# Kernel tuning notes

Hardware: AMD Instinct MI355X
Metric: run time of the kernel (lower is better)

The kernel has to match this reference:

```python
import jax, jax.numpy as jnp
import numpy as np

B, S, D = 16, 2048, 128
NEG = -1000000000.0


def setup_inputs() -> dict:
    key = jax.random.key(0)
    kq, kk, kv = jax.random.split(key, 3)
    q = jax.random.normal(kq, (B, S, D), dtype=jnp.float32)
    k = jax.random.normal(kk, (B, S, D), dtype=jnp.float32)
    v = jax.random.normal(kv, (B, S, D), dtype=jnp.float32)
    # causal mask: True entries are masked out (filled with -1e9)
    mask = jnp.broadcast_to(
        jnp.triu(jnp.ones((S, S), dtype=bool), k=1)[None, :, :], (B, S, S)
    )
    return {"q": q, "k": k, "v": v, "mask": mask}


def reference(q, k, v, mask):
    # attn = q @ k^T / sqrt(d_k), masked_fill, softmax over keys, attn @ v
    scale = jnp.sqrt(jnp.asarray(D, dtype=q.dtype))
    attn = jnp.einsum("bqd,bkd->bqk", q, k) / scale
    attn = jnp.where(mask, jnp.asarray(NEG, dtype=attn.dtype), attn)
    attn = jax.nn.softmax(attn, axis=2)
    out = jnp.einsum("bqk,bkd->bqd", attn, v)
    return (out, attn)
```

## Files before the change

kernel.cpp:

```cpp
#include <hip/hip_runtime.h>

#define B_ 16
#define S_ 2048
#define D_ 128

typedef __attribute__((ext_vector_type(8))) short bf16x8;
typedef __attribute__((ext_vector_type(4))) float f32x4;
typedef __attribute__((ext_vector_type(16))) float f32x16;
typedef __attribute__((ext_vector_type(2))) unsigned int u32x2;
typedef __attribute__((ext_vector_type(4))) unsigned int u32x4;

__device__ __forceinline__ unsigned short f2bf(float f) {
    unsigned int u = __builtin_bit_cast(unsigned int, f);
    u += 0x7fff + ((u >> 16) & 1);
    return (unsigned short)(u >> 16);
}

__device__ __forceinline__ void gload16(const void* g, void* l) {
    __builtin_amdgcn_global_load_lds(
        (const __attribute__((address_space(1))) void*)g,
        (__attribute__((address_space(3))) void*)l, 16, 0, 0);
}

#define WAITV(n) asm volatile("s_waitcnt vmcnt(" #n ")" ::: "memory")

__global__ __launch_bounds__(256, 4)
void conv_kv(const float* __restrict__ kg, const float* __restrict__ vg,
             char* __restrict__ kws, char* __restrict__ vws, float* __restrict__ attng)
{
    __shared__ float lt[64 * 132];
    const int bid = blockIdx.x;
    const int tid = threadIdx.x;
    if (bid < 512) {
        const int b = bid >> 5, t = bid & 31;
        const float* src = kg + ((long)bid << 13);
        char* dst = kws + ((long)bid << 14);
#pragma unroll
        for (int it = 0; it < 4; ++it) {
            const int c = tid + it * 256;
            const int r = c >> 4, j = c & 15;
            f32x4 a = *(const f32x4*)(src + r * 128 + j * 8);
            f32x4 cc = *(const f32x4*)(src + r * 128 + j * 8 + 4);
            u32x4 p;
            p[0] = (unsigned)f2bf(a[0]) | ((unsigned)f2bf(a[1]) << 16);
            p[1] = (unsigned)f2bf(a[2]) | ((unsigned)f2bf(a[3]) << 16);
            p[2] = (unsigned)f2bf(cc[0]) | ((unsigned)f2bf(cc[1]) << 16);
            p[3] = (unsigned)f2bf(cc[2]) | ((unsigned)f2bf(cc[3]) << 16);
            *(u32x4*)(dst + r * 256 + ((j ^ (r & 7)) << 4)) = p;
        }
        const f32x4 z = {0.f, 0.f, 0.f, 0.f};
        {
            const int W4 = (31 - t) * 16;
            float* base = attng + ((long)(b * S_) + t * 64) * S_ + (t + 1) * 64;
            for (int row = 0; row < 32; ++row) {
                float* rb = base + (long)row * S_;
                for (int c = tid; c < W4; c += 256)
                    *(f32x4*)(rb + c * 4) = z;
            }
        }
        {
            const int s = 31 - t;
            const int W4 = t * 16;
            float* base = attng + ((long)(b * S_) + s * 64 + 32) * S_ + (s + 1) * 64;
            for (int row = 0; row < 32; ++row) {
                float* rb = base + (long)row * S_;
                for (int c = tid; c < W4; c += 256)
                    *(f32x4*)(rb + c * 4) = z;
            }
        }
    } else {
        const int vb = bid - 512;
        const float* src = vg + ((long)vb << 13);
        char* dst = vws + ((long)vb << 14);
#pragma unroll
        for (int it = 0; it < 8; ++it) {
            const int c = tid + it * 256;
            const int r = c >> 5, q = c & 31;
            *(f32x4*)(lt + r * 132 + q * 4) = *(const f32x4*)(src + r * 128 + q * 4);
        }
        __syncthreads();
#pragma unroll
        for (int it = 0; it < 4; ++it) {
            const int c = tid + it * 256;
            const int d = c >> 3, jc = c & 7;
            unsigned short e[8];
#pragma unroll
            for (int ee = 0; ee < 8; ++ee) e[ee] = f2bf(lt[(jc * 8 + ee) * 132 + d]);
            u32x4 p;
            p[0] = (unsigned)e[0] | ((unsigned)e[1] << 16);
            p[1] = (unsigned)e[2] | ((unsigned)e[3] << 16);
            p[2] = (unsigned)e[4] | ((unsigned)e[5] << 16);
            p[3] = (unsigned)e[6] | ((unsigned)e[7] << 16);
            *(u32x4*)(dst + d * 128 + ((jc ^ (d & 7)) << 4)) = p;
        }
    }
}

__device__ __forceinline__ int qtile_of(int b, int t) {
    const int f = (t & 1) ? (t >> 1) : (31 - (t >> 1));
    return (b & 8) ? (31 - f) : f;
}

__global__ __launch_bounds__(256, 2)
void flash_fused(const float* __restrict__ qg, const char* __restrict__ kws,
                 const char* __restrict__ vws,
                 float* __restrict__ outg, float* __restrict__ attng)
{
    __shared__ char lds[65536];

    const int tid = threadIdx.x, lane = tid & 63, w = tid >> 6;
    const int wq = w >> 1, wk = w & 1;
    const int l31 = lane & 31, hi = lane >> 5;
    const int bid = blockIdx.x;
    const int b = bid >> 5;
    const int qt = qtile_of(b, bid & 31);
    const int q0 = qt * 64;
    const int nt = qt + 1;
    const float scale = 0.088388347648318447f;
    const int qrow = q0 + wq * 32 + l31;

    bf16x8 qf[8];
    {
        const float* qr = qg + ((long)b * S_ + qrow) * D_;
#pragma unroll
        for (int km = 0; km < 8; ++km) {
            const int d0 = km * 16 + hi * 8;
            f32x4 a = *(const f32x4*)(qr + d0);
            f32x4 c = *(const f32x4*)(qr + d0 + 4);
            bf16x8 t;
            t[0] = (short)f2bf(a[0]); t[1] = (short)f2bf(a[1]);
            t[2] = (short)f2bf(a[2]); t[3] = (short)f2bf(a[3]);
            t[4] = (short)f2bf(c[0]); t[5] = (short)f2bf(c[1]);
            t[6] = (short)f2bf(c[2]); t[7] = (short)f2bf(c[3]);
            qf[km] = t;
        }
    }
    WAITV(0);

    const char* kb0 = kws + ((long)(b * 32) << 14);
    const char* vb0 = vws + ((long)(b * 32) << 14);

    const int krow = wk * 32 + l31;
    const int krb = krow * 256;
    const int ksw = krow & 7;

#pragma unroll
    for (int it = 0; it < 4; ++it)
        gload16(kb0 + it * 4096 + tid * 16, lds + it * 4096 + tid * 16);

    float sumA = 0.f;
    int buf = 0;
    for (int kt = 0; kt < nt; ++kt) {
        const bool pf = (kt + 1 < nt);
        if (pf) {
            const char* kn = kb0 + ((long)(kt + 1) << 14);
            const int db = (buf ^ 1) * 16384;
#pragma unroll
            for (int it = 0; it < 4; ++it)
                gload16(kn + it * 4096 + tid * 16, lds + db + it * 4096 + tid * 16);
            WAITV(4);
        } else {
            WAITV(0);
        }
        __builtin_amdgcn_s_barrier();
        __builtin_amdgcn_sched_barrier(0);

        const char* kbuf = lds + buf * 16384;
        f32x16 acc;
#pragma unroll
        for (int i = 0; i < 16; ++i) acc[i] = 0.f;
        __builtin_amdgcn_s_setprio(1);
#pragma unroll
        for (int km = 0; km < 8; ++km) {
            bf16x8 kf = *(const bf16x8*)(kbuf + krb + (((km * 2 + hi) ^ ksw) << 4));
            acc = __builtin_amdgcn_mfma_f32_32x32x16_bf16(kf, qf[km], acc, 0, 0, 0);
        }
        __builtin_amdgcn_s_setprio(0);

        const int kbase = kt * 64 + wk * 32;
#pragma unroll
        for (int r = 0; r < 16; ++r) {
            const int kl = (r & 3) + 8 * (r >> 2) + 4 * hi;
            if (kbase + kl <= qrow) sumA += __expf(acc[r] * scale);
        }
        __builtin_amdgcn_sched_barrier(0);
        __builtin_amdgcn_s_barrier();
        buf ^= 1;
    }

    sumA += __shfl_xor(sumA, 32, 64);
    float* sums = (float*)lds;
    if (!hi) sums[(wq * 2 + wk) * 32 + l31] = sumA;
    __syncthreads();
    const float invl_l = 1.f / (sums[(wq * 2 + 0) * 32 + l31] + sums[(wq * 2 + 1) * 32 + l31]);
    __syncthreads();

    f32x16 oacc[4];
#pragma unroll
    for (int dt = 0; dt < 4; ++dt)
#pragma unroll
        for (int i = 0; i < 16; ++i) oacc[dt][i] = 0.f;

    float* attn_row = attng + ((long)b * S_ + qrow) * S_;

#pragma unroll
    for (int it = 0; it < 4; ++it)
        gload16(kb0 + it * 4096 + tid * 16, lds + it * 4096 + tid * 16);
#pragma unroll
    for (int it = 0; it < 4; ++it)
        gload16(vb0 + it * 4096 + tid * 16, lds + 32768 + it * 4096 + tid * 16);

    buf = 0;
    for (int kt = 0; kt < nt; ++kt) {
        const bool pf = (kt + 1 < nt);
        if (pf) {
            const char* kn = kb0 + ((long)(kt + 1) << 14);
            const char* vn = vb0 + ((long)(kt + 1) << 14);
            const int db = (buf ^ 1) * 16384;
#pragma unroll
            for (int it = 0; it < 4; ++it)
                gload16(kn + it * 4096 + tid * 16, lds + db + it * 4096 + tid * 16);
#pragma unroll
            for (int it = 0; it < 4; ++it)
                gload16(vn + it * 4096 + tid * 16, lds + 32768 + db + it * 4096 + tid * 16);
        }
        if (kt == 0) { if (pf) { WAITV(8); } else { WAITV(0); } }
        else         { if (pf) { WAITV(12); } else { WAITV(4); } }
        __builtin_amdgcn_s_barrier();
        __builtin_amdgcn_sched_barrier(0);

        const char* kbuf = lds + buf * 16384;
        const char* vbuf = lds + 32768 + buf * 16384;

        f32x16 acc;
#pragma unroll
        for (int i = 0; i < 16; ++i) acc[i] = 0.f;
        __builtin_amdgcn_s_setprio(1);
#pragma unroll
        for (int km = 0; km < 8; ++km) {
            bf16x8 kf = *(const bf16x8*)(kbuf + krb + (((km * 2 + hi) ^ ksw) << 4));
            acc = __builtin_amdgcn_mfma_f32_32x32x16_bf16(kf, qf[km], acc, 0, 0, 0);
        }
        __builtin_amdgcn_s_setprio(0);

        const int kbase = kt * 64 + wk * 32;
        unsigned W[8], PW[8];
#pragma unroll
        for (int i = 0; i < 8; ++i) {
            const int r0 = 2 * i;
            const int kl0 = (r0 & 3) + 8 * (r0 >> 2) + 4 * hi;
            const float p0 = (kbase + kl0 > qrow) ? 0.f : __expf(acc[r0] * scale);
            const float p1 = (kbase + kl0 + 1 > qrow) ? 0.f : __expf(acc[r0 + 1] * scale);
            W[i] = (unsigned)f2bf(p0) | ((unsigned)f2bf(p1) << 16);
        }
#pragma unroll
        for (int i = 0; i < 8; ++i)
            PW[i] = (unsigned)__shfl_xor((int)W[i], 32, 64);

        bf16x8 pa[2];
        float* arow = attn_row + kbase;
#pragma unroll
        for (int kc = 0; kc < 2; ++kc) {
            u32x4 fr;
            fr[0] = hi ? PW[kc * 4 + 2] : W[kc * 4 + 0];
            fr[1] = hi ? PW[kc * 4 + 3] : W[kc * 4 + 1];
            fr[2] = hi ? W[kc * 4 + 2] : PW[kc * 4 + 0];
            fr[3] = hi ? W[kc * 4 + 3] : PW[kc * 4 + 1];
            pa[kc] = __builtin_bit_cast(bf16x8, fr);
            f32x4 s0, s1;
            s0[0] = __builtin_bit_cast(float, fr[0] << 16) * invl_l;
            s0[1] = __builtin_bit_cast(float, fr[0] & 0xffff0000u) * invl_l;
            s0[2] = __builtin_bit_cast(float, fr[1] << 16) * invl_l;
            s0[3] = __builtin_bit_cast(float, fr[1] & 0xffff0000u) * invl_l;
            s1[0] = __builtin_bit_cast(float, fr[2] << 16) * invl_l;
            s1[1] = __builtin_bit_cast(float, fr[2] & 0xffff0000u) * invl_l;
            s1[2] = __builtin_bit_cast(float, fr[3] << 16) * invl_l;
            s1[3] = __builtin_bit_cast(float, fr[3] & 0xffff0000u) * invl_l;
            *(f32x4*)(arow + kc * 16 + hi * 8) = s0;
            *(f32x4*)(arow + kc * 16 + hi * 8 + 4) = s1;
        }

        __builtin_amdgcn_s_setprio(1);
#pragma unroll
        for (int dt = 0; dt < 4; ++dt) {
            const int d = dt * 32 + l31;
            const int rowb = d * 128;
            const int sw = (d & 7) << 4;
#pragma unroll
            for (int kc = 0; kc < 2; ++kc) {
                const int jc = wk * 4 + kc * 2 + hi;
                bf16x8 vf = *(const bf16x8*)(vbuf + rowb + ((jc << 4) ^ sw));
                oacc[dt] = __builtin_amdgcn_mfma_f32_32x32x16_bf16(pa[kc], vf, oacc[dt], 0, 0, 0);
            }
        }
        __builtin_amdgcn_s_setprio(0);
        __builtin_amdgcn_sched_barrier(0);
        __builtin_amdgcn_s_barrier();
        buf ^= 1;
    }

    __syncthreads();
    float* red = (float*)lds;
    if (wk) {
#pragma unroll
        for (int dt = 0; dt < 4; ++dt)
#pragma unroll
            for (int r = 0; r < 16; ++r) {
                const int qr = (r & 3) + 8 * (r >> 2) + 4 * hi;
                red[wq * 4096 + qr * 128 + dt * 32 + l31] = oacc[dt][r];
            }
    }
    __syncthreads();
    if (!wk) {
        float iv[16];
#pragma unroll
        for (int r = 0; r < 16; ++r) {
            const int qr = (r & 3) + 8 * (r >> 2) + 4 * hi;
            iv[r] = __shfl(invl_l, qr, 64);
        }
        float* ob = outg + ((long)b * S_ + q0 + wq * 32) * D_;
#pragma unroll
        for (int dt = 0; dt < 4; ++dt)
#pragma unroll
            for (int r = 0; r < 16; ++r) {
                const int qr = (r & 3) + 8 * (r >> 2) + 4 * hi;
                ob[(long)qr * D_ + dt * 32 + l31] =
                    (oacc[dt][r] + red[wq * 4096 + qr * 128 + dt * 32 + l31]) * iv[r];
            }
    }
}

__global__ __launch_bounds__(256, 2)
void attn_fallback(const float* __restrict__ qg, const float* __restrict__ kg,
                   const float* __restrict__ vg,
                   float* __restrict__ outg, float* __restrict__ attng)
{
    __shared__ unsigned short kT[64 * 128];
    __shared__ unsigned short vT[128 * 64];
    __shared__ unsigned short pT[4][16 * 64];
    const int tid = threadIdx.x, lane = tid & 63, w = tid >> 6;
    const int l15 = lane & 15, l4 = lane >> 4;
    const int bid = blockIdx.x;
    const int b = bid >> 5, qt = 31 - (bid & 31), q0 = qt * 64;
    const float scale = 0.088388347648318447f;
    bf16x8 qf[4];
    {
        const float* qrow = qg + ((long)b * S_ + q0 + w * 16 + l15) * D_;
#pragma unroll
        for (int kk = 0; kk < 4; ++kk) {
            const int d0 = kk * 32 + l4 * 8;
            f32x4 a = *(const f32x4*)(qrow + d0);
            f32x4 c = *(const f32x4*)(qrow + d0 + 4);
            bf16x8 t;
            t[0] = (short)f2bf(a[0]); t[1] = (short)f2bf(a[1]);
            t[2] = (short)f2bf(a[2]); t[3] = (short)f2bf(a[3]);
            t[4] = (short)f2bf(c[0]); t[5] = (short)f2bf(c[1]);
            t[6] = (short)f2bf(c[2]); t[7] = (short)f2bf(c[3]);
            qf[kk] = t;
        }
    }
    float m[4], l[4];
#pragma unroll
    for (int r = 0; r < 4; ++r) { m[r] = -1e30f; l[r] = 0.f; }
    for (int kt = 0; kt <= qt; ++kt) {
        __syncthreads();
        {
            const float* kbase = kg + ((long)b * S_ + kt * 64) * D_;
#pragma unroll
            for (int it = 0; it < 8; ++it) {
                const int c = tid + it * 256, row = c >> 5, dc = c & 31;
                f32x4 a = *(const f32x4*)(kbase + row * D_ + dc * 4);
                u32x2 p;
                p[0] = (unsigned)f2bf(a[0]) | ((unsigned)f2bf(a[1]) << 16);
                p[1] = (unsigned)f2bf(a[2]) | ((unsigned)f2bf(a[3]) << 16);
                *(u32x2*)((char*)kT + row * 256 + ((dc * 8) ^ ((row & 7) << 4))) = p;
            }
        }
        __syncthreads();
        f32x4 acc[4];
#pragma unroll
        for (int n = 0; n < 4; ++n) {
            f32x4 a = {0.f, 0.f, 0.f, 0.f};
            const int krow = n * 16 + l15, rb = krow * 256, swz = (krow & 7) << 4;
#pragma unroll
            for (int kk = 0; kk < 4; ++kk) {
                bf16x8 bf = *(const bf16x8*)((const char*)kT + rb + ((l4 * 16 + kk * 64) ^ swz));
                a = __builtin_amdgcn_mfma_f32_16x16x32_bf16(qf[kk], bf, a, 0, 0, 0);
            }
            acc[n] = a;
        }
        const bool diag = (kt == qt);
        float tm[4] = {-3e38f, -3e38f, -3e38f, -3e38f};
#pragma unroll
        for (int n = 0; n < 4; ++n)
#pragma unroll
            for (int r = 0; r < 4; ++r) {
                float s = acc[n][r] * scale;
                if (diag && (n * 16 + l15 > w * 16 + l4 * 4 + r)) s = -3e38f;
                acc[n][r] = s; tm[r] = fmaxf(tm[r], s);
            }
#pragma unroll
        for (int off = 1; off < 16; off <<= 1)
#pragma unroll
            for (int r = 0; r < 4; ++r) tm[r] = fmaxf(tm[r], __shfl_xor(tm[r], off, 64));
        float sum[4], mn[4];
#pragma unroll
        for (int r = 0; r < 4; ++r) {
            mn[r] = fmaxf(m[r], tm[r]);
            float s0 = 0.f;
#pragma unroll
            for (int n = 0; n < 4; ++n) s0 += __expf(acc[n][r] - mn[r]);
            sum[r] = s0;
        }
#pragma unroll
        for (int off = 1; off < 16; off <<= 1)
#pragma unroll
            for (int r = 0; r < 4; ++r) sum[r] += __shfl_xor(sum[r], off, 64);
#pragma unroll
        for (int r = 0; r < 4; ++r) { l[r] = l[r] * __expf(m[r] - mn[r]) + sum[r]; m[r] = mn[r]; }
    }
    float invl[4];
#pragma unroll
    for (int r = 0; r < 4; ++r) invl[r] = 1.f / l[r];
    f32x4 oacc[8];
#pragma unroll
    for (int n = 0; n < 8; ++n) oacc[n] = (f32x4){0.f, 0.f, 0.f, 0.f};
    float* attn_base = attng + ((long)b * S_ + q0) * S_;
    for (int kt = 0; kt <= qt; ++kt) {
        __syncthreads();
        {
            const float* kbase = kg + ((long)b * S_ + kt * 64) * D_;
#pragma unroll
            for (int it = 0; it < 8; ++it) {
                const int c = tid + it * 256, row = c >> 5, dc = c & 31;
                f32x4 a = *(const f32x4*)(kbase + row * D_ + dc * 4);
                u32x2 p;
                p[0] = (unsigned)f2bf(a[0]) | ((unsigned)f2bf(a[1]) << 16);
                p[1] = (unsigned)f2bf(a[2]) | ((unsigned)f2bf(a[3]) << 16);
                *(u32x2*)((char*)kT + row * 256 + ((dc * 8) ^ ((row & 7) << 4))) = p;
            }
        }
        {
            const float* vbase = vg + ((long)b * S_ + kt * 64) * D_;
#pragma unroll
            for (int it = 0; it < 8; ++it) {
                const int c = tid + it * 256, kr = c & 63, dq = c >> 6;
                f32x4 a = *(const f32x4*)(vbase + kr * D_ + dq * 4);
#pragma unroll
                for (int j = 0; j < 4; ++j) {
                    const int d = dq * 4 + j;
                    *(unsigned short*)((char*)vT + d * 128 + ((kr * 2) ^ ((d & 7) << 4))) = f2bf(a[j]);
                }
            }
        }
        __syncthreads();
        f32x4 acc[4];
#pragma unroll
        for (int n = 0; n < 4; ++n) {
            f32x4 a = {0.f, 0.f, 0.f, 0.f};
            const int krow = n * 16 + l15, rb = krow * 256, swz = (krow & 7) << 4;
#pragma unroll
            for (int kk = 0; kk < 4; ++kk) {
                bf16x8 bf = *(const bf16x8*)((const char*)kT + rb + ((l4 * 16 + kk * 64) ^ swz));
                a = __builtin_amdgcn_mfma_f32_16x16x32_bf16(qf[kk], bf, a, 0, 0, 0);
            }
            acc[n] = a;
        }
        const bool diag = (kt == qt);
#pragma unroll
        for (int n = 0; n < 4; ++n)
#pragma unroll
            for (int r = 0; r < 4; ++r) {
                float s = acc[n][r] * scale;
                if (diag && (n * 16 + l15 > w * 16 + l4 * 4 + r)) s = -3e38f;
                const float p = __expf(s - m[r]) * invl[r];
                attn_base[(long)(w * 16 + l4 * 4 + r) * S_ + kt * 64 + n * 16 + l15] = p;
                const int prow = l4 * 4 + r;
                *(unsigned short*)((char*)&pT[w][0] + prow * 128 + ((n * 32 + l15 * 2) ^ ((prow & 7) << 4))) = f2bf(p);
            }
        asm volatile("s_waitcnt lgkmcnt(0)" ::: "memory");
        __builtin_amdgcn_sched_barrier(0);
        bf16x8 pa[2];
#pragma unroll
        for (int kk = 0; kk < 2; ++kk)
            pa[kk] = *(const bf16x8*)((const char*)&pT[w][0] + l15 * 128 + ((l4 * 16 + kk * 64) ^ ((l15 & 7) << 4)));
#pragma unroll
        for (int n = 0; n < 8; ++n) {
            const int vrow = n * 16 + l15, rb = vrow * 128, swz = (vrow & 7) << 4;
#pragma unroll
            for (int kk = 0; kk < 2; ++kk) {
                bf16x8 bv = *(const bf16x8*)((const char*)vT + rb + ((l4 * 16 + kk * 64) ^ swz));
                oacc[n] = __builtin_amdgcn_mfma_f32_16x16x32_bf16(pa[kk], bv, oacc[n], 0, 0, 0);
            }
        }
    }
    {
        float* obase = outg + ((long)b * S_ + q0 + w * 16) * D_;
#pragma unroll
        for (int n = 0; n < 8; ++n)
#pragma unroll
            for (int r = 0; r < 4; ++r)
                obase[(long)(l4 * 4 + r) * D_ + n * 16 + l15] = oacc[n][r];
    }
    {
        const int col0 = (qt + 1) * 64;
        if (col0 < S_) {
            const int nch = (S_ - col0) >> 2;
            const f32x4 z = {0.f, 0.f, 0.f, 0.f};
            for (int row = w; row < 64; row += 4) {
                float* rbase = attn_base + (long)row * S_ + col0;
                for (int c = lane; c < nch; c += 64)
                    *(f32x4*)(rbase + c * 4) = z;
            }
        }
    }
}

extern "C" void kernel_launch(void* const* d_in, const int* in_sizes, int n_in,
                              void* d_out, int out_size, void* d_ws, size_t ws_size,
                              hipStream_t stream) {
    const float* q = (const float*)d_in[0];
    const float* k = (const float*)d_in[1];
    const float* v = (const float*)d_in[2];
    float* out  = (float*)d_out;
    float* attn = out + (long)B_ * S_ * D_;
    const size_t NEED = 2u * 8388608u;
    if (ws_size >= NEED) {
        char* kws = (char*)d_ws;
        char* vws = kws + 8388608;
        conv_kv<<<dim3(1024), dim3(256), 0, stream>>>(k, v, kws, vws, attn);
        flash_fused<<<dim3(512), dim3(256), 0, stream>>>(q, kws, vws, out, attn);
    } else {
        attn_fallback<<<dim3(512), dim3(256), 0, stream>>>(q, k, v, out, attn);
    }
}
```

Before: 122.3 us.

## Single-pass flash with unnormalized bf16 P workspace and separate expand kernel

Replaces the two-pass attention (a QK pass for row sums, then a second QK pass that writes normalized attn and accumulates PV) with one pass. That pass stores the unnormalized bf16 probabilities to a workspace, accumulates PV, and writes the per-row inverse sums. A new expand kernel then reads the bf16 P, scales it by the inverse sum and writes the fp32 attn matrix. This removes the redundant QK^T recompute and K reload. In exchange it adds an extra workspace write and read of P and a third kernel launch, and the new path is used only when the workspace is large enough.

```diff
diff --git a/kernel.cpp b/kernel.cpp
--- a/kernel.cpp
+++ b/kernel.cpp
@@ -23,6 +23,8 @@
 }
 
 #define WAITV(n) asm volatile("s_waitcnt vmcnt(" #n ")" ::: "memory")
+
+#define PB 4325376L
 
 __global__ __launch_bounds__(256, 4)
 void conv_kv(const float* __restrict__ kg, const float* __restrict__ vg,
@@ -102,9 +104,9 @@
 }
 
 __global__ __launch_bounds__(256, 2)
-void flash_fused(const float* __restrict__ qg, const char* __restrict__ kws,
-                 const char* __restrict__ vws,
-                 float* __restrict__ outg, float* __restrict__ attng)
+void flash_p(const float* __restrict__ qg, const char* __restrict__ kws,
+             const char* __restrict__ vws, float* __restrict__ lg,
+             char* __restrict__ pws, float* __restrict__ outg)
 {
     __shared__ char lds[65536];
 
@@ -118,6 +120,7 @@
     const int nt = qt + 1;
     const float scale = 0.088388347648318447f;
     const int qrow = q0 + wq * 32 + l31;
+    const int lr = wq * 32 + l31;
 
     bf16x8 qf[8];
     {
@@ -137,8 +140,17 @@
     }
     WAITV(0);
 
+    f32x16 oacc[4];
+#pragma unroll
+    for (int dt = 0; dt < 4; ++dt)
+#pragma unroll
+        for (int i = 0; i < 16; ++i) oacc[dt][i] = 0.f;
+    float sumA = 0.f;
+
     const char* kb0 = kws + ((long)(b * 32) << 14);
     const char* vb0 = vws + ((long)(b * 32) << 14);
+    char* pbase = pws + (long)b * PB + 4096L * qt * (qt + 1);
+    const int prstride = nt * 128;
 
     const int krow = wk * 32 + l31;
     const int krb = krow * 256;
@@ -147,7 +159,204 @@
 #pragma unroll
     for (int it = 0; it < 4; ++it)
         gload16(kb0 + it * 4096 + tid * 16, lds + it * 4096 + tid * 16);
-
+#pragma unroll
+    for (int it = 0; it < 4; ++it)
+        gload16(vb0 + it * 4096 + tid * 16, lds + 32768 + it * 4096 + tid * 16);
+
+    int buf = 0;
+    for (int kt = 0; kt < nt; ++kt) {
+        const bool pf = (kt + 1 < nt);
+        if (pf) {
+            const char* kn = kb0 + ((long)(kt + 1) << 14);
+            const char* vn = vb0 + ((long)(kt + 1) << 14);
+            const int db = (buf ^ 1) * 16384;
+#pragma unroll
+            for (int it = 0; it < 4; ++it)
+                gload16(kn + it * 4096 + tid * 16, lds + db + it * 4096 + tid * 16);
+#pragma unroll
+            for (int it = 0; it < 4; ++it)
+                gload16(vn + it * 4096 + tid * 16, lds + 32768 + db + it * 4096 + tid * 16);
+        }
+        if (kt == 0) { if (pf) { WAITV(8); } else { WAITV(0); } }
+        else         { if (pf) { WAITV(10); } else { WAITV(2); } }
+        __builtin_amdgcn_s_barrier();
+        __builtin_amdgcn_sched_barrier(0);
+
+        const char* kbuf = lds + buf * 16384;
+        const char* vbuf = lds + 32768 + buf * 16384;
+
+        f32x16 acc;
+#pragma unroll
+        for (int i = 0; i < 16; ++i) acc[i] = 0.f;
+        __builtin_amdgcn_s_setprio(1);
+#pragma unroll
+        for (int km = 0; km < 8; ++km) {
+            bf16x8 kf = *(const bf16x8*)(kbuf + krb + (((km * 2 + hi) ^ ksw) << 4));
+            acc = __builtin_amdgcn_mfma_f32_32x32x16_bf16(kf, qf[km], acc, 0, 0, 0);
+        }
+        __builtin_amdgcn_s_setprio(0);
+
+        const int kbase = kt * 64 + wk * 32;
+        unsigned W[8], PW[8];
+#pragma unroll
+        for (int i = 0; i < 8; ++i) {
+            const int r0 = 2 * i;
+            const int kl0 = (r0 & 3) + 8 * (r0 >> 2) + 4 * hi;
+            const float p0 = (kbase + kl0 > qrow) ? 0.f : __expf(acc[r0] * scale);
+            const float p1 = (kbase + kl0 + 1 > qrow) ? 0.f : __expf(acc[r0 + 1] * scale);
+            sumA += p0 + p1;
+            W[i] = (unsigned)f2bf(p0) | ((unsigned)f2bf(p1) << 16);
+        }
+#pragma unroll
+        for (int i = 0; i < 8; ++i)
+            PW[i] = (unsigned)__shfl_xor((int)W[i], 32, 64);
+
+        bf16x8 pa[2];
+#pragma unroll
+        for (int kc = 0; kc < 2; ++kc) {
+            u32x4 fr;
+            fr[0] = hi ? PW[kc * 4 + 2] : W[kc * 4 + 0];
+            fr[1] = hi ? PW[kc * 4 + 3] : W[kc * 4 + 1];
+            fr[2] = hi ? W[kc * 4 + 2] : PW[kc * 4 + 0];
+            fr[3] = hi ? W[kc * 4 + 3] : PW[kc * 4 + 1];
+            pa[kc] = __builtin_bit_cast(bf16x8, fr);
+            const int col = kbase + kc * 16 + hi * 8;
+            *(u32x4*)(pbase + (long)lr * prstride + col * 2) = fr;
+        }
+
+        __builtin_amdgcn_s_setprio(1);
+#pragma unroll
+        for (int dt = 0; dt < 4; ++dt) {
+            const int d = dt * 32 + l31;
+            const int rowb = d * 128;
+            const int sw = (d & 7) << 4;
+#pragma unroll
+            for (int kc = 0; kc < 2; ++kc) {
+                const int jc = wk * 4 + kc * 2 + hi;
+                bf16x8 vf = *(const bf16x8*)(vbuf + rowb + ((jc << 4) ^ sw));
+                oacc[dt] = __builtin_amdgcn_mfma_f32_32x32x16_bf16(pa[kc], vf, oacc[dt], 0, 0, 0);
+            }
+        }
+        __builtin_amdgcn_s_setprio(0);
+        __builtin_amdgcn_sched_barrier(0);
+        __builtin_amdgcn_s_barrier();
+        buf ^= 1;
+    }
+
+    sumA += __shfl_xor(sumA, 32, 64);
+    __syncthreads();
+    float* sums = (float*)lds;
+    if (!hi) sums[(wq * 2 + wk) * 32 + l31] = sumA;
+    __syncthreads();
+    const float invl_l = 1.f / (sums[(wq * 2 + 0) * 32 + l31] + sums[(wq * 2 + 1) * 32 + l31]);
+    if (wk == 0 && !hi) lg[(long)b * S_ + qrow] = invl_l;
+    __syncthreads();
+
+    float* red = (float*)lds;
+    if (wk) {
+#pragma unroll
+        for (int dt = 0; dt < 4; ++dt)
+#pragma unroll
+            for (int r = 0; r < 16; ++r) {
+                const int qr = (r & 3) + 8 * (r >> 2) + 4 * hi;
+                red[wq * 4096 + qr * 128 + dt * 32 + l31] = oacc[dt][r];
+            }
+    }
+    __syncthreads();
+    if (!wk) {
+        float iv[16];
+#pragma unroll
+        for (int r = 0; r < 16; ++r) {
+            const int qr = (r & 3) + 8 * (r >> 2) + 4 * hi;
+            iv[r] = __shfl(invl_l, qr, 64);
+        }
+        float* ob = outg + ((long)b * S_ + q0 + wq * 32) * D_;
+#pragma unroll
+        for (int dt = 0; dt < 4; ++dt)
+#pragma unroll
+            for (int r = 0; r < 16; ++r) {
+                const int qr = (r & 3) + 8 * (r >> 2) + 4 * hi;
+                ob[(long)qr * D_ + dt * 32 + l31] =
+                    (oacc[dt][r] + red[wq * 4096 + qr * 128 + dt * 32 + l31]) * iv[r];
+            }
+    }
+}
+
+__global__ __launch_bounds__(256, 4)
+void expand(const char* __restrict__ pws, const float* __restrict__ lg,
+            float* __restrict__ attng)
+{
+    const int tid = threadIdx.x;
+    const int bid = blockIdx.x;
+    const int b = bid >> 5;
+    const int qt = qtile_of(b, bid & 31);
+    const int q0 = qt * 64;
+    const int nt = qt + 1;
+    const int w8 = nt * 8;
+    const char* pbase = pws + (long)b * PB + 4096L * qt * (qt + 1);
+
+    for (int row = 0; row < 64; ++row) {
+        const float invl = lg[(long)b * S_ + q0 + row];
+        const char* pr = pbase + (long)row * nt * 128;
+        float* ar = attng + ((long)b * S_ + q0 + row) * S_;
+        for (int c = tid; c < w8; c += 256) {
+            u32x4 pk = *(const u32x4*)(pr + c * 16);
+            f32x4 o0, o1;
+            o0[0] = __builtin_bit_cast(float, pk[0] << 16) * invl;
+            o0[1] = __builtin_bit_cast(float, pk[0] & 0xffff0000u) * invl;
+            o0[2] = __builtin_bit_cast(float, pk[1] << 16) * invl;
+            o0[3] = __builtin_bit_cast(float, pk[1] & 0xffff0000u) * invl;
+            o1[0] = __builtin_bit_cast(float, pk[2] << 16) * invl;
+            o1[1] = __builtin_bit_cast(float, pk[2] & 0xffff0000u) * invl;
+            o1[2] = __builtin_bit_cast(float, pk[3] << 16) * invl;
+            o1[3] = __builtin_bit_cast(float, pk[3] & 0xffff0000u) * invl;
+            *(f32x4*)(ar + c * 8) = o0;
+            *(f32x4*)(ar + c * 8 + 4) = o1;
+        }
+    }
+}
+
+__global__ __launch_bounds__(256, 2)
+void flash_fused(const float* __restrict__ qg, const char* __restrict__ kws,
+                 const char* __restrict__ vws,
+                 float* __restrict__ outg, float* __restrict__ attng)
+{
+    __shared__ char lds[65536];
+    const int tid = threadIdx.x, lane = tid & 63, w = tid >> 6;
+    const int wq = w >> 1, wk = w & 1;
+    const int l31 = lane & 31, hi = lane >> 5;
+    const int bid = blockIdx.x;
+    const int b = bid >> 5;
+    const int qt = qtile_of(b, bid & 31);
+    const int q0 = qt * 64;
+    const int nt = qt + 1;
+    const float scale = 0.088388347648318447f;
+    const int qrow = q0 + wq * 32 + l31;
+    bf16x8 qf[8];
+    {
+        const float* qr = qg + ((long)b * S_ + qrow) * D_;
+#pragma unroll
+        for (int km = 0; km < 8; ++km) {
+            const int d0 = km * 16 + hi * 8;
+            f32x4 a = *(const f32x4*)(qr + d0);
+            f32x4 c = *(const f32x4*)(qr + d0 + 4);
+            bf16x8 t;
+            t[0] = (short)f2bf(a[0]); t[1] = (short)f2bf(a[1]);
+            t[2] = (short)f2bf(a[2]); t[3] = (short)f2bf(a[3]);
+            t[4] = (short)f2bf(c[0]); t[5] = (short)f2bf(c[1]);
+            t[6] = (short)f2bf(c[2]); t[7] = (short)f2bf(c[3]);
+            qf[km] = t;
+        }
+    }
+    WAITV(0);
+    const char* kb0 = kws + ((long)(b * 32) << 14);
+    const char* vb0 = vws + ((long)(b * 32) << 14);
+    const int krow = wk * 32 + l31;
+    const int krb = krow * 256;
+    const int ksw = krow & 7;
+#pragma unroll
+    for (int it = 0; it < 4; ++it)
+        gload16(kb0 + it * 4096 + tid * 16, lds + it * 4096 + tid * 16);
     float sumA = 0.f;
     int buf = 0;
     for (int kt = 0; kt < nt; ++kt) {
@@ -159,12 +368,9 @@
             for (int it = 0; it < 4; ++it)
                 gload16(kn + it * 4096 + tid * 16, lds + db + it * 4096 + tid * 16);
             WAITV(4);
-        } else {
-            WAITV(0);
-        }
+        } else { WAITV(0); }
         __builtin_amdgcn_s_barrier();
         __builtin_amdgcn_sched_barrier(0);
-
         const char* kbuf = lds + buf * 16384;
         f32x16 acc;
 #pragma unroll
@@ -176,7 +382,6 @@
             acc = __builtin_amdgcn_mfma_f32_32x32x16_bf16(kf, qf[km], acc, 0, 0, 0);
         }
         __builtin_amdgcn_s_setprio(0);
-
         const int kbase = kt * 64 + wk * 32;
 #pragma unroll
         for (int r = 0; r < 16; ++r) {
@@ -187,29 +392,24 @@
         __builtin_amdgcn_s_barrier();
         buf ^= 1;
     }
-
     sumA += __shfl_xor(sumA, 32, 64);
     float* sums = (float*)lds;
     if (!hi) sums[(wq * 2 + wk) * 32 + l31] = sumA;
     __syncthreads();
     const float invl_l = 1.f / (sums[(wq * 2 + 0) * 32 + l31] + sums[(wq * 2 + 1) * 32 + l31]);
     __syncthreads();
-
     f32x16 oacc[4];
 #pragma unroll
     for (int dt = 0; dt < 4; ++dt)
 #pragma unroll
         for (int i = 0; i < 16; ++i) oacc[dt][i] = 0.f;
-
     float* attn_row = attng + ((long)b * S_ + qrow) * S_;
-
 #pragma unroll
     for (int it = 0; it < 4; ++it)
         gload16(kb0 + it * 4096 + tid * 16, lds + it * 4096 + tid * 16);
 #pragma unroll
     for (int it = 0; it < 4; ++it)
         gload16(vb0 + it * 4096 + tid * 16, lds + 32768 + it * 4096 + tid * 16);
-
     buf = 0;
     for (int kt = 0; kt < nt; ++kt) {
         const bool pf = (kt + 1 < nt);
@@ -228,10 +428,8 @@
         else         { if (pf) { WAITV(12); } else { WAITV(4); } }
         __builtin_amdgcn_s_barrier();
         __builtin_amdgcn_sched_barrier(0);
-
         const char* kbuf = lds + buf * 16384;
         const char* vbuf = lds + 32768 + buf * 16384;
-
         f32x16 acc;
 #pragma unroll
         for (int i = 0; i < 16; ++i) acc[i] = 0.f;
@@ -242,7 +440,6 @@
             acc = __builtin_amdgcn_mfma_f32_32x32x16_bf16(kf, qf[km], acc, 0, 0, 0);
         }
         __builtin_amdgcn_s_setprio(0);
-
         const int kbase = kt * 64 + wk * 32;
         unsigned W[8], PW[8];
 #pragma unroll
@@ -256,7 +453,6 @@
 #pragma unroll
         for (int i = 0; i < 8; ++i)
             PW[i] = (unsigned)__shfl_xor((int)W[i], 32, 64);
-
         bf16x8 pa[2];
         float* arow = attn_row + kbase;
 #pragma unroll
@@ -279,7 +475,6 @@
             *(f32x4*)(arow + kc * 16 + hi * 8) = s0;
             *(f32x4*)(arow + kc * 16 + hi * 8 + 4) = s1;
         }
-
         __builtin_amdgcn_s_setprio(1);
 #pragma unroll
         for (int dt = 0; dt < 4; ++dt) {
@@ -298,7 +493,6 @@
         __builtin_amdgcn_s_barrier();
         buf ^= 1;
     }
-
     __syncthreads();
     float* red = (float*)lds;
     if (wk) {
@@ -524,10 +718,20 @@
     const float* v = (const float*)d_in[2];
     float* out  = (float*)d_out;
     float* attn = out + (long)B_ * S_ * D_;
-    const size_t NEED = 2u * 8388608u;
-    if (ws_size >= NEED) {
+    const size_t LG = 131072, KV = 8388608;
+    const size_t NEED_BIG = LG + 2 * KV + (size_t)PB * B_;
+    const size_t NEED_MID = 2 * KV;
+    if (ws_size >= NEED_BIG) {
+        float* lg = (float*)d_ws;
+        char* kws = (char*)d_ws + LG;
+        char* vws = kws + KV;
+        char* pws = vws + KV;
+        conv_kv<<<dim3(1024), dim3(256), 0, stream>>>(k, v, kws, vws, attn);
+        flash_p<<<dim3(512), dim3(256), 0, stream>>>(q, kws, vws, lg, pws, out);
+        expand<<<dim3(512), dim3(256), 0, stream>>>(pws, lg, attn);
+    } else if (ws_size >= NEED_MID) {
         char* kws = (char*)d_ws;
-        char* vws = kws + 8388608;
+        char* vws = kws + KV;
         conv_kv<<<dim3(1024), dim3(256), 0, stream>>>(k, v, kws, vws, attn);
         flash_fused<<<dim3(512), dim3(256), 0, stream>>>(q, kws, vws, out, attn);
     } else {
```

After: 127.2 us. 1.04x slower.

## Move causal zero-fill into attention kernel, split QK accumulators, issue PV MFMAs before stores

Applied to the files above, without the earlier changes.

Writing zeros into the masked upper-triangle region of the attention matrix moves from the K/V conversion kernel to the tail of the fused attention kernel, so each block clears the columns past its last key tile. The QK^T MFMA chain now alternates between two accumulators to shorten the dependent chain, at the cost of an extra add per element. The P·V MFMAs are issued before the global stores of the normalized probabilities, so matrix math can overlap the store traffic. Together these rebalance memory writes across kernels and expose more instruction-level parallelism, while adding register pressure.

```diff
diff --git a/kernel.cpp b/kernel.cpp
--- a/kernel.cpp
+++ b/kernel.cpp
@@ -26,13 +26,12 @@
 
 __global__ __launch_bounds__(256, 4)
 void conv_kv(const float* __restrict__ kg, const float* __restrict__ vg,
-             char* __restrict__ kws, char* __restrict__ vws, float* __restrict__ attng)
+             char* __restrict__ kws, char* __restrict__ vws)
 {
     __shared__ float lt[64 * 132];
     const int bid = blockIdx.x;
     const int tid = threadIdx.x;
     if (bid < 512) {
-        const int b = bid >> 5, t = bid & 31;
         const float* src = kg + ((long)bid << 13);
         char* dst = kws + ((long)bid << 14);
 #pragma unroll
@@ -48,26 +47,6 @@
             p[3] = (unsigned)f2bf(cc[2]) | ((unsigned)f2bf(cc[3]) << 16);
             *(u32x4*)(dst + r * 256 + ((j ^ (r & 7)) << 4)) = p;
         }
-        const f32x4 z = {0.f, 0.f, 0.f, 0.f};
-        {
-            const int W4 = (31 - t) * 16;
-            float* base = attng + ((long)(b * S_) + t * 64) * S_ + (t + 1) * 64;
-            for (int row = 0; row < 32; ++row) {
-                float* rb = base + (long)row * S_;
-                for (int c = tid; c < W4; c += 256)
-                    *(f32x4*)(rb + c * 4) = z;
-            }
-        }
-        {
-            const int s = 31 - t;
-            const int W4 = t * 16;
-            float* base = attng + ((long)(b * S_) + s * 64 + 32) * S_ + (s + 1) * 64;
-            for (int row = 0; row < 32; ++row) {
-                float* rb = base + (long)row * S_;
-                for (int c = tid; c < W4; c += 256)
-                    *(f32x4*)(rb + c * 4) = z;
-            }
-        }
     } else {
         const int vb = bid - 512;
         const float* src = vg + ((long)vb << 13);
@@ -139,7 +118,6 @@
 
     const char* kb0 = kws + ((long)(b * 32) << 14);
     const char* vb0 = vws + ((long)(b * 32) << 14);
-
     const int krow = wk * 32 + l31;
     const int krb = krow * 256;
     const int ksw = krow & 7;
@@ -159,21 +137,20 @@
             for (int it = 0; it < 4; ++it)
                 gload16(kn + it * 4096 + tid * 16, lds + db + it * 4096 + tid * 16);
             WAITV(4);
-        } else {
-            WAITV(0);
-        }
+        } else { WAITV(0); }
         __builtin_amdgcn_s_barrier();
         __builtin_amdgcn_sched_barrier(0);
 
         const char* kbuf = lds + buf * 16384;
-        f32x16 acc;
-#pragma unroll
-        for (int i = 0; i < 16; ++i) acc[i] = 0.f;
+        f32x16 a0, a1;
+#pragma unroll
+        for (int i = 0; i < 16; ++i) { a0[i] = 0.f; a1[i] = 0.f; }
         __builtin_amdgcn_s_setprio(1);
 #pragma unroll
         for (int km = 0; km < 8; ++km) {
             bf16x8 kf = *(const bf16x8*)(kbuf + krb + (((km * 2 + hi) ^ ksw) << 4));
-            acc = __builtin_amdgcn_mfma_f32_32x32x16_bf16(kf, qf[km], acc, 0, 0, 0);
+            if (km & 1) a1 = __builtin_amdgcn_mfma_f32_32x32x16_bf16(kf, qf[km], a1, 0, 0, 0);
+            else        a0 = __builtin_amdgcn_mfma_f32_32x32x16_bf16(kf, qf[km], a0, 0, 0, 0);
         }
         __builtin_amdgcn_s_setprio(0);
 
@@ -181,7 +158,7 @@
 #pragma unroll
         for (int r = 0; r < 16; ++r) {
             const int kl = (r & 3) + 8 * (r >> 2) + 4 * hi;
-            if (kbase + kl <= qrow) sumA += __expf(acc[r] * scale);
+            if (kbase + kl <= qrow) sumA += __expf((a0[r] + a1[r]) * scale);
         }
         __builtin_amdgcn_sched_barrier(0);
         __builtin_amdgcn_s_barrier();
@@ -232,14 +209,15 @@
         const char* kbuf = lds + buf * 16384;
         const char* vbuf = lds + 32768 + buf * 16384;
 
-        f32x16 acc;
-#pragma unroll
-        for (int i = 0; i < 16; ++i) acc[i] = 0.f;
+        f32x16 a0, a1;
+#pragma unroll
+        for (int i = 0; i < 16; ++i) { a0[i] = 0.f; a1[i] = 0.f; }
         __builtin_amdgcn_s_setprio(1);
 #pragma unroll
         for (int km = 0; km < 8; ++km) {
             bf16x8 kf = *(const bf16x8*)(kbuf + krb + (((km * 2 + hi) ^ ksw) << 4));
-            acc = __builtin_amdgcn_mfma_f32_32x32x16_bf16(kf, qf[km], acc, 0, 0, 0);
+            if (km & 1) a1 = __builtin_amdgcn_mfma_f32_32x32x16_bf16(kf, qf[km], a1, 0, 0, 0);
+            else        a0 = __builtin_amdgcn_mfma_f32_32x32x16_bf16(kf, qf[km], a0, 0, 0, 0);
         }
         __builtin_amdgcn_s_setprio(0);
 
@@ -249,8 +227,8 @@
         for (int i = 0; i < 8; ++i) {
             const int r0 = 2 * i;
             const int kl0 = (r0 & 3) + 8 * (r0 >> 2) + 4 * hi;
-            const float p0 = (kbase + kl0 > qrow) ? 0.f : __expf(acc[r0] * scale);
-            const float p1 = (kbase + kl0 + 1 > qrow) ? 0.f : __expf(acc[r0 + 1] * scale);
+            const float p0 = (kbase + kl0 > qrow) ? 0.f : __expf((a0[r0] + a1[r0]) * scale);
+            const float p1 = (kbase + kl0 + 1 > qrow) ? 0.f : __expf((a0[r0 + 1] + a1[r0 + 1]) * scale);
             W[i] = (unsigned)f2bf(p0) | ((unsigned)f2bf(p1) << 16);
         }
 #pragma unroll
@@ -258,7 +236,7 @@
             PW[i] = (unsigned)__shfl_xor((int)W[i], 32, 64);
 
         bf16x8 pa[2];
-        float* arow = attn_row + kbase;
+        u32x4 frs[2];
 #pragma unroll
         for (int kc = 0; kc < 2; ++kc) {
             u32x4 fr;
@@ -266,7 +244,29 @@
             fr[1] = hi ? PW[kc * 4 + 3] : W[kc * 4 + 1];
             fr[2] = hi ? W[kc * 4 + 2] : PW[kc * 4 + 0];
             fr[3] = hi ? W[kc * 4 + 3] : PW[kc * 4 + 1];
+            frs[kc] = fr;
             pa[kc] = __builtin_bit_cast(bf16x8, fr);
+        }
+
+        __builtin_amdgcn_s_setprio(1);
+#pragma unroll
+        for (int dt = 0; dt < 4; ++dt) {
+            const int d = dt * 32 + l31;
+            const int rowb = d * 128;
+            const int sw = (d & 7) << 4;
+#pragma unroll
+            for (int kc = 0; kc < 2; ++kc) {
+                const int jc = wk * 4 + kc * 2 + hi;
+                bf16x8 vf = *(const bf16x8*)(vbuf + rowb + ((jc << 4) ^ sw));
+                oacc[dt] = __builtin_amdgcn_mfma_f32_32x32x16_bf16(pa[kc], vf, oacc[dt], 0, 0, 0);
+            }
+        }
+        __builtin_amdgcn_s_setprio(0);
+
+        float* arow = attn_row + kbase;
+#pragma unroll
+        for (int kc = 0; kc < 2; ++kc) {
+            const u32x4 fr = frs[kc];
             f32x4 s0, s1;
             s0[0] = __builtin_bit_cast(float, fr[0] << 16) * invl_l;
             s0[1] = __builtin_bit_cast(float, fr[0] & 0xffff0000u) * invl_l;
@@ -279,21 +279,6 @@
             *(f32x4*)(arow + kc * 16 + hi * 8) = s0;
             *(f32x4*)(arow + kc * 16 + hi * 8 + 4) = s1;
         }
-
-        __builtin_amdgcn_s_setprio(1);
-#pragma unroll
-        for (int dt = 0; dt < 4; ++dt) {
-            const int d = dt * 32 + l31;
-            const int rowb = d * 128;
-            const int sw = (d & 7) << 4;
-#pragma unroll
-            for (int kc = 0; kc < 2; ++kc) {
-                const int jc = wk * 4 + kc * 2 + hi;
-                bf16x8 vf = *(const bf16x8*)(vbuf + rowb + ((jc << 4) ^ sw));
-                oacc[dt] = __builtin_amdgcn_mfma_f32_32x32x16_bf16(pa[kc], vf, oacc[dt], 0, 0, 0);
-            }
-        }
-        __builtin_amdgcn_s_setprio(0);
         __builtin_amdgcn_sched_barrier(0);
         __builtin_amdgcn_s_barrier();
         buf ^= 1;
@@ -327,6 +312,20 @@
                 ob[(long)qr * D_ + dt * 32 + l31] =
                     (oacc[dt][r] + red[wq * 4096 + qr * 128 + dt * 32 + l31]) * iv[r];
             }
+    }
+
+    {
+        const int col0 = nt * 64;
+        if (col0 < S_) {
+            const int nch = (S_ - col0) >> 2;
+            const f32x4 z = {0.f, 0.f, 0.f, 0.f};
+            float* fb = attng + ((long)b * S_ + q0) * S_ + col0;
+            for (int row = w; row < 64; row += 4) {
+                float* rb = fb + (long)row * S_;
+                for (int c = lane; c < nch; c += 64)
+                    *(f32x4*)(rb + c * 4) = z;
+            }
+        }
     }
 }
 
@@ -528,7 +527,7 @@
     if (ws_size >= NEED) {
         char* kws = (char*)d_ws;
         char* vws = kws + 8388608;
-        conv_kv<<<dim3(1024), dim3(256), 0, stream>>>(k, v, kws, vws, attn);
+        conv_kv<<<dim3(1024), dim3(256), 0, stream>>>(k, v, kws, vws);
         flash_fused<<<dim3(512), dim3(256), 0, stream>>>(q, kws, vws, out, attn);
     } else {
         attn_fallback<<<dim3(512), dim3(256), 0, stream>>>(q, k, v, out, attn);
```

Result: faster. 117.4 us (-4.0%).
